# Performance work log

Hardware: AMD Instinct MI355X
Metric: run time of the kernel (lower is better)

Reference implementation:

```python
import jax, jax.numpy as jnp
import numpy as np

T, C, H = 2048, 1024, 16
D = C // H  # head dim = 64


def setup_inputs() -> dict:
    key = jax.random.key(0)
    k1, k2, k3 = jax.random.split(key, 3)
    x = jax.random.normal(k1, (T, C), dtype=jnp.float32)
    W_qkv = jax.random.normal(k2, (C, 3 * C), dtype=jnp.float32) * (1.0 / np.sqrt(C))
    b_qkv = jnp.zeros((3 * C,), dtype=jnp.float32)
    W_proj = jax.random.normal(k3, (C, C), dtype=jnp.float32) * (1.0 / np.sqrt(C))
    b_proj = jnp.zeros((C,), dtype=jnp.float32)
    return {"x": x, "W_qkv": W_qkv, "b_qkv": b_qkv, "W_proj": W_proj, "b_proj": b_proj}


def reference(x, W_qkv, b_qkv, W_proj, b_proj):
    t, c = x.shape
    qkv = x @ W_qkv + b_qkv                      # [T, 3C] fused QKV projection
    q, k, v = jnp.split(qkv, 3, axis=-1)         # each [T, C]
    # split heads: [T, C] -> [H, T, D]
    q = q.reshape(t, H, D).transpose(1, 0, 2)
    k = k.reshape(t, H, D).transpose(1, 0, 2)
    v = v.reshape(t, H, D).transpose(1, 0, 2)
    # naive O(T^2) attention, full score matrix [H, T, T]
    att = jnp.einsum('htd,hsd->hts', q, k) / jnp.sqrt(jnp.float32(D))
    att = jax.nn.softmax(att, axis=-1)
    y = jnp.einsum('hts,hsd->htd', att, v)       # [H, T, D]
    y = y.transpose(1, 0, 2).reshape(t, c)       # merge heads -> [T, C]
    return y @ W_proj + b_proj
```

## Files before the change

kernel.cpp:

```cpp
#include <hip/hip_runtime.h>
#include <hip/hip_bf16.h>
#include <stdint.h>

#define T_DIM 2048
#define C_DIM 1024
#define H_DIM 16
#define D_HEAD 64
#define N_QKV 3072

typedef __bf16 bf16;
typedef __bf16 bf16x8 __attribute__((ext_vector_type(8)));
typedef __bf16 bf16x4 __attribute__((ext_vector_type(4)));
typedef float f32x4 __attribute__((ext_vector_type(4)));

__global__ void cast_bf16_kernel(const float* __restrict__ in, bf16* __restrict__ out, int n) {
    int i = (blockIdx.x * 256 + threadIdx.x) * 8;
    if (i >= n) return;
    float4 a = *(const float4*)(in + i);
    float4 b = *(const float4*)(in + i + 4);
    bf16x8 o;
    o[0] = (bf16)a.x; o[1] = (bf16)a.y; o[2] = (bf16)a.z; o[3] = (bf16)a.w;
    o[4] = (bf16)b.x; o[5] = (bf16)b.y; o[6] = (bf16)b.z; o[7] = (bf16)b.w;
    *(bf16x8*)(out + i) = o;
}

__global__ void cast_transpose_kernel(const float* __restrict__ in, bf16* __restrict__ out,
                                      int K, int N) {
    __shared__ float tile[32][33];
    int kb = blockIdx.y * 32, nb = blockIdx.x * 32;
    int t = threadIdx.x;
    int r = t >> 3, c4 = (t & 7) * 4;
    float4 v = *(const float4*)(in + (size_t)(kb + r) * N + nb + c4);
    tile[r][c4 + 0] = v.x; tile[r][c4 + 1] = v.y;
    tile[r][c4 + 2] = v.z; tile[r][c4 + 3] = v.w;
    __syncthreads();
    bf16x4 ov;
    ov[0] = (bf16)tile[c4 + 0][r]; ov[1] = (bf16)tile[c4 + 1][r];
    ov[2] = (bf16)tile[c4 + 2][r]; ov[3] = (bf16)tile[c4 + 3][r];
    *(bf16x4*)(out + (size_t)(nb + r) * K + kb + c4) = ov;
}

template <typename OutT>
__global__ __launch_bounds__(256, 2) void gemm_bt_kernel(
    const bf16* __restrict__ A, const bf16* __restrict__ Bt,
    const float* __restrict__ bias, OutT* __restrict__ Cmat,
    int M, int N, int K)
{
    __shared__ __align__(16) bf16 As[128][40];
    __shared__ __align__(16) bf16 Bs[128][40];
    int tid  = threadIdx.x;
    int lane = tid & 63, w = tid >> 6;
    int lo16 = lane & 15, quad = lane >> 4;
    int wm = (w & 1) * 64, wn = (w >> 1) * 64;
    int rowBase = blockIdx.y * 128, colBase = blockIdx.x * 128;

    const bf16* aRow = A  + (size_t)(rowBase + (tid >> 1)) * K + (tid & 1) * 16;
    const bf16* bRow = Bt + (size_t)(colBase + (tid >> 1)) * K + (tid & 1) * 16;
    bf16* asDst = &As[tid >> 1][(tid & 1) * 16];
    bf16* bsDst = &Bs[tid >> 1][(tid & 1) * 16];

    f32x4 acc[4][4] = {};

    for (int k0 = 0; k0 < K; k0 += 32) {
        bf16x8 a0 = *(const bf16x8*)(aRow + k0);
        bf16x8 a1 = *(const bf16x8*)(aRow + k0 + 8);
        bf16x8 b0 = *(const bf16x8*)(bRow + k0);
        bf16x8 b1 = *(const bf16x8*)(bRow + k0 + 8);
        __syncthreads();
        *(bf16x8*)asDst = a0; *(bf16x8*)(asDst + 8) = a1;
        *(bf16x8*)bsDst = b0; *(bf16x8*)(bsDst + 8) = b1;
        __syncthreads();
        bf16x8 af[4], bfr[4];
        #pragma unroll
        for (int mi = 0; mi < 4; ++mi) af[mi]  = *(const bf16x8*)&As[wm + mi * 16 + lo16][quad * 8];
        #pragma unroll
        for (int ni = 0; ni < 4; ++ni) bfr[ni] = *(const bf16x8*)&Bs[wn + ni * 16 + lo16][quad * 8];
        #pragma unroll
        for (int mi = 0; mi < 4; ++mi)
            #pragma unroll
            for (int ni = 0; ni < 4; ++ni)
                acc[mi][ni] = __builtin_amdgcn_mfma_f32_16x16x32_bf16(af[mi], bfr[ni], acc[mi][ni], 0, 0, 0);
    }

    #pragma unroll
    for (int ni = 0; ni < 4; ++ni) {
        int col = colBase + wn + ni * 16 + lo16;
        float bv = bias[col];
        #pragma unroll
        for (int mi = 0; mi < 4; ++mi) {
            int row0 = rowBase + wm + mi * 16 + quad * 4;
            #pragma unroll
            for (int r = 0; r < 4; ++r) {
                float v = acc[mi][ni][r] + bv;
                Cmat[(size_t)(row0 + r) * N + col] = (OutT)v;
            }
        }
    }
}

__global__ __launch_bounds__(256, 2) void gemm_bt_128x64_kernel(
    const bf16* __restrict__ A, const bf16* __restrict__ Bt,
    const float* __restrict__ bias, float* __restrict__ Cmat,
    int M, int N, int K)
{
    __shared__ __align__(16) bf16 As[128][40];
    __shared__ __align__(16) bf16 Bs[64][40];
    int tid  = threadIdx.x;
    int lane = tid & 63, w = tid >> 6;
    int lo16 = lane & 15, quad = lane >> 4;
    int wm = (w & 1) * 64, wn = (w >> 1) * 32;
    int rowBase = blockIdx.y * 128, colBase = blockIdx.x * 64;

    const bf16* aRow = A  + (size_t)(rowBase + (tid >> 1)) * K + (tid & 1) * 16;
    const bf16* bRow = Bt + (size_t)(colBase + (tid >> 2)) * K + (tid & 3) * 8;
    bf16* asDst = &As[tid >> 1][(tid & 1) * 16];
    bf16* bsDst = &Bs[tid >> 2][(tid & 3) * 8];

    f32x4 acc[4][2] = {};

    for (int k0 = 0; k0 < K; k0 += 32) {
        bf16x8 a0 = *(const bf16x8*)(aRow + k0);
        bf16x8 a1 = *(const bf16x8*)(aRow + k0 + 8);
        bf16x8 b0 = *(const bf16x8*)(bRow + k0);
        __syncthreads();
        *(bf16x8*)asDst = a0; *(bf16x8*)(asDst + 8) = a1;
        *(bf16x8*)bsDst = b0;
        __syncthreads();
        bf16x8 af[4], bfr[2];
        #pragma unroll
        for (int mi = 0; mi < 4; ++mi) af[mi]  = *(const bf16x8*)&As[wm + mi * 16 + lo16][quad * 8];
        #pragma unroll
        for (int ni = 0; ni < 2; ++ni) bfr[ni] = *(const bf16x8*)&Bs[wn + ni * 16 + lo16][quad * 8];
        #pragma unroll
        for (int mi = 0; mi < 4; ++mi)
            #pragma unroll
            for (int ni = 0; ni < 2; ++ni)
                acc[mi][ni] = __builtin_amdgcn_mfma_f32_16x16x32_bf16(af[mi], bfr[ni], acc[mi][ni], 0, 0, 0);
    }

    #pragma unroll
    for (int ni = 0; ni < 2; ++ni) {
        int col = colBase + wn + ni * 16 + lo16;
        float bv = bias[col];
        #pragma unroll
        for (int mi = 0; mi < 4; ++mi) {
            int row0 = rowBase + wm + mi * 16 + quad * 4;
            #pragma unroll
            for (int r = 0; r < 4; ++r)
                Cmat[(size_t)(row0 + r) * N + col] = acc[mi][ni][r] + bv;
        }
    }
}

__global__ __launch_bounds__(256) void flash_kernel(
    const bf16* __restrict__ qkv,
    bf16* __restrict__ y)
{
    __shared__ __align__(16) bf16 Kd[2][64][40];
    __shared__ __align__(16) bf16 Vt[2][64][40];
    __shared__ __align__(16) bf16 Ps[4][16][72];

    const int h = blockIdx.x, qb = blockIdx.y;
    const int tid  = threadIdx.x;
    const int lane = tid & 63, w = tid >> 6;
    const int lo16 = lane & 15, quad = lane >> 4;
    const int qrow0 = qb * 64 + w * 16;

    bf16x8 qf[2];
    #pragma unroll
    for (int dk = 0; dk < 2; ++dk)
        qf[dk] = *(const bf16x8*)(qkv + (size_t)(qrow0 + lo16) * N_QKV + h * D_HEAD + dk * 32 + quad * 8);

    f32x4 o[4] = {};
    f32x4 l_acc = {};

    const int krow = tid >> 3, kch = tid & 7;
    const int kh = kch >> 2, kc = kch & 3;
    const bf16* kbase = qkv + C_DIM + h * D_HEAD;
    const unsigned short* vbase16 = (const unsigned short*)(qkv + 2 * C_DIM + h * D_HEAD);
    const int vkk = w >> 1, vsb = (w & 1) * 16;

    bf16x8 kreg0, kreg1;
    unsigned short vreg[16];

    {
        const bf16* kp = kbase + (size_t)krow * N_QKV + kch * 8;
        kreg0 = *(const bf16x8*)kp;
        kreg1 = *(const bf16x8*)(kp + (size_t)32 * N_QKV);
        #pragma unroll
        for (int i = 0; i < 16; ++i)
            vreg[i] = vbase16[(size_t)(w * 16 + i) * N_QKV + lane];
    }

    for (int kt = 0; kt < T_DIM / 64; ++kt) {
        __syncthreads();
        *(bf16x8*)&Kd[kh][krow][kc * 8]      = kreg0;
        *(bf16x8*)&Kd[kh][krow + 32][kc * 8] = kreg1;
        union { bf16x8 v; unsigned short u[8]; } p0, p1;
        #pragma unroll
        for (int i = 0; i < 8; ++i) { p0.u[i] = vreg[i]; p1.u[i] = vreg[8 + i]; }
        *(bf16x8*)&Vt[vkk][lane][vsb]     = p0.v;
        *(bf16x8*)&Vt[vkk][lane][vsb + 8] = p1.v;
        __syncthreads();

        if (kt + 1 < T_DIM / 64) {
            const bf16* kp = kbase + (size_t)((kt + 1) * 64 + krow) * N_QKV + kch * 8;
            kreg0 = *(const bf16x8*)kp;
            kreg1 = *(const bf16x8*)(kp + (size_t)32 * N_QKV);
            #pragma unroll
            for (int i = 0; i < 16; ++i)
                vreg[i] = vbase16[(size_t)((kt + 1) * 64 + w * 16 + i) * N_QKV + lane];
        }

        f32x4 s[4] = {};
        #pragma unroll
        for (int dk = 0; dk < 2; ++dk)
            #pragma unroll
            for (int ni = 0; ni < 4; ++ni) {
                bf16x8 kf = *(const bf16x8*)&Kd[dk][ni * 16 + lo16][quad * 8];
                s[ni] = __builtin_amdgcn_mfma_f32_16x16x32_bf16(qf[dk], kf, s[ni], 0, 0, 0);
            }

        #pragma unroll
        for (int ni = 0; ni < 4; ++ni)
            #pragma unroll
            for (int r = 0; r < 4; ++r) {
                float p = __builtin_amdgcn_exp2f(s[ni][r] * 0.18033688011112042f);
                l_acc[r] += p;
                Ps[w][quad * 4 + r][ni * 16 + lo16] = (bf16)p;
            }

        bf16x8 pa0 = *(const bf16x8*)&Ps[w][lo16][quad * 8];
        bf16x8 pa1 = *(const bf16x8*)&Ps[w][lo16][32 + quad * 8];

        #pragma unroll
        for (int ni = 0; ni < 4; ++ni) {
            bf16x8 v0 = *(const bf16x8*)&Vt[0][ni * 16 + lo16][quad * 8];
            o[ni] = __builtin_amdgcn_mfma_f32_16x16x32_bf16(pa0, v0, o[ni], 0, 0, 0);
        }
        #pragma unroll
        for (int ni = 0; ni < 4; ++ni) {
            bf16x8 v1 = *(const bf16x8*)&Vt[1][ni * 16 + lo16][quad * 8];
            o[ni] = __builtin_amdgcn_mfma_f32_16x16x32_bf16(pa1, v1, o[ni], 0, 0, 0);
        }
    }

    #pragma unroll
    for (int off = 1; off < 16; off <<= 1)
        #pragma unroll
        for (int r = 0; r < 4; ++r) l_acc[r] += __shfl_xor(l_acc[r], off);

    f32x4 linv;
    #pragma unroll
    for (int r = 0; r < 4; ++r) linv[r] = 1.0f / l_acc[r];
    #pragma unroll
    for (int ni = 0; ni < 4; ++ni)
        #pragma unroll
        for (int r = 0; r < 4; ++r)
            y[(size_t)(qrow0 + quad * 4 + r) * C_DIM + h * D_HEAD + ni * 16 + lo16] =
                (bf16)(o[ni][r] * linv[r]);
}

extern "C" void kernel_launch(void* const* d_in, const int* in_sizes, int n_in,
                              void* d_out, int out_size, void* d_ws, size_t ws_size,
                              hipStream_t stream) {
    const float* x      = (const float*)d_in[0];
    const float* W_qkv  = (const float*)d_in[1];
    const float* b_qkv  = (const float*)d_in[2];
    const float* W_proj = (const float*)d_in[3];
    const float* b_proj = (const float*)d_in[4];
    float* out = (float*)d_out;

    char* ws = (char*)d_ws;
    bf16* xb      = (bf16*)(ws);
    bf16* Wqkv_t  = (bf16*)(ws + (4  << 20));
    bf16* Wproj_t = (bf16*)(ws + (10 << 20));
    bf16* qkv_bf  = (bf16*)(ws + (12 << 20));
    bf16* yb      = (bf16*)(ws + (24 << 20));

    cast_bf16_kernel<<<(T_DIM * C_DIM) / (256 * 8), 256, 0, stream>>>(x, xb, T_DIM * C_DIM);
    cast_transpose_kernel<<<dim3(N_QKV / 32, C_DIM / 32), 256, 0, stream>>>(W_qkv, Wqkv_t, C_DIM, N_QKV);
    cast_transpose_kernel<<<dim3(C_DIM / 32, C_DIM / 32), 256, 0, stream>>>(W_proj, Wproj_t, C_DIM, C_DIM);

    gemm_bt_kernel<bf16><<<dim3(N_QKV / 128, T_DIM / 128), 256, 0, stream>>>(
        xb, Wqkv_t, b_qkv, qkv_bf, T_DIM, N_QKV, C_DIM);

    flash_kernel<<<dim3(H_DIM, T_DIM / 64), 256, 0, stream>>>(qkv_bf, yb);

    gemm_bt_128x64_kernel<<<dim3(C_DIM / 64, T_DIM / 128), 256, 0, stream>>>(
        yb, Wproj_t, b_proj, out, T_DIM, C_DIM, C_DIM);
}
```

Measured before the change: 174.4 us.

## Split KV in flash attention, add combine pass, use direct-to-LDS GEMM loads

The attention kernel now splits the key/value sequence into two halves across a third grid dimension. It computes transposed S^T and O^T tiles with each wave owning a KV slice, then reduces partial outputs across waves in LDS, and a new combine kernel merges the two halves. Both GEMMs are replaced by a single 128x64 kernel that uses global_load_lds to copy tiles straight into unpadded shared memory. The aim is more parallelism in attention and less register traffic in the GEMMs. The cost is extra partial-output memory traffic, a new kernel launch, and possible LDS bank conflicts from removing the padding.

```diff
diff --git a/kernel.cpp b/kernel.cpp
--- a/kernel.cpp
+++ b/kernel.cpp
@@ -12,6 +12,27 @@
 typedef __bf16 bf16x8 __attribute__((ext_vector_type(8)));
 typedef __bf16 bf16x4 __attribute__((ext_vector_type(4)));
 typedef float f32x4 __attribute__((ext_vector_type(4)));
+typedef short s16x4 __attribute__((ext_vector_type(4)));
+
+__device__ __forceinline__ void lds_load16(const void* g, void* l) {
+    __builtin_amdgcn_global_load_lds(
+        (const __attribute__((address_space(1))) void*)g,
+        (__attribute__((address_space(3))) void*)l, 16, 0, 0);
+}
+
+__device__ __forceinline__ f32x4 mfma16(bf16x4 a, bf16x4 b, f32x4 c) {
+#if __has_builtin(__builtin_amdgcn_mfma_f32_16x16x16_bf16)
+    return __builtin_amdgcn_mfma_f32_16x16x16_bf16(a, b, c, 0, 0, 0);
+#elif __has_builtin(__builtin_amdgcn_mfma_f32_16x16x16bf16_1k)
+    union { bf16x4 v; s16x4 s; } ua, ub;
+    ua.v = a; ub.v = b;
+    return __builtin_amdgcn_mfma_f32_16x16x16bf16_1k(ua.s, ub.s, c, 0, 0, 0);
+#else
+    asm volatile("v_mfma_f32_16x16x16_bf16 %0, %1, %2, %0"
+                 : "+v"(c) : "v"(a), "v"(b));
+    return c;
+#endif
+}
 
 __global__ void cast_bf16_kernel(const float* __restrict__ in, bf16* __restrict__ out, int n) {
     int i = (blockIdx.x * 256 + threadIdx.x) * 8;
@@ -41,90 +62,32 @@
 }
 
 template <typename OutT>
-__global__ __launch_bounds__(256, 2) void gemm_bt_kernel(
+__global__ __launch_bounds__(256) void gemm_lds_kernel(
     const bf16* __restrict__ A, const bf16* __restrict__ Bt,
     const float* __restrict__ bias, OutT* __restrict__ Cmat,
     int M, int N, int K)
 {
-    __shared__ __align__(16) bf16 As[128][40];
-    __shared__ __align__(16) bf16 Bs[128][40];
-    int tid  = threadIdx.x;
-    int lane = tid & 63, w = tid >> 6;
-    int lo16 = lane & 15, quad = lane >> 4;
-    int wm = (w & 1) * 64, wn = (w >> 1) * 64;
-    int rowBase = blockIdx.y * 128, colBase = blockIdx.x * 128;
-
-    const bf16* aRow = A  + (size_t)(rowBase + (tid >> 1)) * K + (tid & 1) * 16;
-    const bf16* bRow = Bt + (size_t)(colBase + (tid >> 1)) * K + (tid & 1) * 16;
-    bf16* asDst = &As[tid >> 1][(tid & 1) * 16];
-    bf16* bsDst = &Bs[tid >> 1][(tid & 1) * 16];
-
-    f32x4 acc[4][4] = {};
-
-    for (int k0 = 0; k0 < K; k0 += 32) {
-        bf16x8 a0 = *(const bf16x8*)(aRow + k0);
-        bf16x8 a1 = *(const bf16x8*)(aRow + k0 + 8);
-        bf16x8 b0 = *(const bf16x8*)(bRow + k0);
-        bf16x8 b1 = *(const bf16x8*)(bRow + k0 + 8);
-        __syncthreads();
-        *(bf16x8*)asDst = a0; *(bf16x8*)(asDst + 8) = a1;
-        *(bf16x8*)bsDst = b0; *(bf16x8*)(bsDst + 8) = b1;
-        __syncthreads();
-        bf16x8 af[4], bfr[4];
-        #pragma unroll
-        for (int mi = 0; mi < 4; ++mi) af[mi]  = *(const bf16x8*)&As[wm + mi * 16 + lo16][quad * 8];
-        #pragma unroll
-        for (int ni = 0; ni < 4; ++ni) bfr[ni] = *(const bf16x8*)&Bs[wn + ni * 16 + lo16][quad * 8];
-        #pragma unroll
-        for (int mi = 0; mi < 4; ++mi)
-            #pragma unroll
-            for (int ni = 0; ni < 4; ++ni)
-                acc[mi][ni] = __builtin_amdgcn_mfma_f32_16x16x32_bf16(af[mi], bfr[ni], acc[mi][ni], 0, 0, 0);
-    }
-
-    #pragma unroll
-    for (int ni = 0; ni < 4; ++ni) {
-        int col = colBase + wn + ni * 16 + lo16;
-        float bv = bias[col];
-        #pragma unroll
-        for (int mi = 0; mi < 4; ++mi) {
-            int row0 = rowBase + wm + mi * 16 + quad * 4;
-            #pragma unroll
-            for (int r = 0; r < 4; ++r) {
-                float v = acc[mi][ni][r] + bv;
-                Cmat[(size_t)(row0 + r) * N + col] = (OutT)v;
-            }
-        }
-    }
-}
-
-__global__ __launch_bounds__(256, 2) void gemm_bt_128x64_kernel(
-    const bf16* __restrict__ A, const bf16* __restrict__ Bt,
-    const float* __restrict__ bias, float* __restrict__ Cmat,
-    int M, int N, int K)
-{
-    __shared__ __align__(16) bf16 As[128][40];
-    __shared__ __align__(16) bf16 Bs[64][40];
+    __shared__ __align__(16) bf16 As[128][32];
+    __shared__ __align__(16) bf16 Bs[64][32];
     int tid  = threadIdx.x;
     int lane = tid & 63, w = tid >> 6;
     int lo16 = lane & 15, quad = lane >> 4;
     int wm = (w & 1) * 64, wn = (w >> 1) * 32;
     int rowBase = blockIdx.y * 128, colBase = blockIdx.x * 64;
 
-    const bf16* aRow = A  + (size_t)(rowBase + (tid >> 1)) * K + (tid & 1) * 16;
-    const bf16* bRow = Bt + (size_t)(colBase + (tid >> 2)) * K + (tid & 3) * 8;
-    bf16* asDst = &As[tid >> 1][(tid & 1) * 16];
-    bf16* bsDst = &Bs[tid >> 2][(tid & 3) * 8];
+    const bf16* ga = A  + (size_t)(rowBase + w * 16 + (lane >> 2)) * K + (lane & 3) * 8;
+    const bf16* gb = Bt + (size_t)(colBase + w * 16 + (lane >> 2)) * K + (lane & 3) * 8;
+    bf16* la0 = &As[w * 16][0];
+    bf16* la1 = &As[64 + w * 16][0];
+    bf16* lb  = &Bs[w * 16][0];
 
     f32x4 acc[4][2] = {};
 
     for (int k0 = 0; k0 < K; k0 += 32) {
-        bf16x8 a0 = *(const bf16x8*)(aRow + k0);
-        bf16x8 a1 = *(const bf16x8*)(aRow + k0 + 8);
-        bf16x8 b0 = *(const bf16x8*)(bRow + k0);
-        __syncthreads();
-        *(bf16x8*)asDst = a0; *(bf16x8*)(asDst + 8) = a1;
-        *(bf16x8*)bsDst = b0;
+        __syncthreads();
+        lds_load16(ga + k0, la0);
+        lds_load16(ga + (size_t)64 * K + k0, la1);
+        lds_load16(gb + k0, lb);
         __syncthreads();
         bf16x8 af[4], bfr[2];
         #pragma unroll
@@ -146,119 +109,158 @@
         for (int mi = 0; mi < 4; ++mi) {
             int row0 = rowBase + wm + mi * 16 + quad * 4;
             #pragma unroll
-            for (int r = 0; r < 4; ++r)
-                Cmat[(size_t)(row0 + r) * N + col] = acc[mi][ni][r] + bv;
-        }
-    }
-}
-
-__global__ __launch_bounds__(256) void flash_kernel(
+            for (int r = 0; r < 4; ++r) {
+                float v = acc[mi][ni][r] + bv;
+                Cmat[(size_t)(row0 + r) * N + col] = (OutT)v;
+            }
+        }
+    }
+}
+
+__global__ __launch_bounds__(256, 3) void flash_kernel(
     const bf16* __restrict__ qkv,
-    bf16* __restrict__ y)
+    bf16* __restrict__ Opart,
+    float* __restrict__ lpart)
 {
-    __shared__ __align__(16) bf16 Kd[2][64][40];
-    __shared__ __align__(16) bf16 Vt[2][64][40];
-    __shared__ __align__(16) bf16 Ps[4][16][72];
-
-    const int h = blockIdx.x, qb = blockIdx.y;
+    __shared__ union {
+        struct {
+            __align__(16) bf16 Kd[2][64][40];
+            __align__(16) bf16 Vt[2][64][40];
+        } t;
+        float Ored[4][16][66];
+    } u;
+    __shared__ float lred[4][64];
+
+    const int h = blockIdx.x, qb = blockIdx.y, sp = blockIdx.z;
     const int tid  = threadIdx.x;
     const int lane = tid & 63, w = tid >> 6;
     const int lo16 = lane & 15, quad = lane >> 4;
-    const int qrow0 = qb * 64 + w * 16;
-
-    bf16x8 qf[2];
-    #pragma unroll
-    for (int dk = 0; dk < 2; ++dk)
-        qf[dk] = *(const bf16x8*)(qkv + (size_t)(qrow0 + lo16) * N_QKV + h * D_HEAD + dk * 32 + quad * 8);
-
-    f32x4 o[4] = {};
-    f32x4 l_acc = {};
+    const int kv0 = sp * (T_DIM / 2);
+
+    bf16x8 qf[4][2];
+    #pragma unroll
+    for (int nq = 0; nq < 4; ++nq)
+        #pragma unroll
+        for (int dk = 0; dk < 2; ++dk)
+            qf[nq][dk] = *(const bf16x8*)(qkv + (size_t)(qb * 64 + nq * 16 + lo16) * N_QKV
+                                          + h * D_HEAD + dk * 32 + quad * 8);
+
+    f32x4 o_t[4][4] = {};
+    float l_acc[4] = {};
 
     const int krow = tid >> 3, kch = tid & 7;
     const int kh = kch >> 2, kc = kch & 3;
     const bf16* kbase = qkv + C_DIM + h * D_HEAD;
-    const unsigned short* vbase16 = (const unsigned short*)(qkv + 2 * C_DIM + h * D_HEAD);
-    const int vkk = w >> 1, vsb = (w & 1) * 16;
+    const unsigned short* vb16 = (const unsigned short*)(qkv + 2 * C_DIM + h * D_HEAD);
 
     bf16x8 kreg0, kreg1;
     unsigned short vreg[16];
-
     {
-        const bf16* kp = kbase + (size_t)krow * N_QKV + kch * 8;
+        const bf16* kp = kbase + (size_t)(kv0 + krow) * N_QKV + kch * 8;
         kreg0 = *(const bf16x8*)kp;
         kreg1 = *(const bf16x8*)(kp + (size_t)32 * N_QKV);
         #pragma unroll
         for (int i = 0; i < 16; ++i)
-            vreg[i] = vbase16[(size_t)(w * 16 + i) * N_QKV + lane];
-    }
-
-    for (int kt = 0; kt < T_DIM / 64; ++kt) {
-        __syncthreads();
-        *(bf16x8*)&Kd[kh][krow][kc * 8]      = kreg0;
-        *(bf16x8*)&Kd[kh][krow + 32][kc * 8] = kreg1;
-        union { bf16x8 v; unsigned short u[8]; } p0, p1;
-        #pragma unroll
-        for (int i = 0; i < 8; ++i) { p0.u[i] = vreg[i]; p1.u[i] = vreg[8 + i]; }
-        *(bf16x8*)&Vt[vkk][lane][vsb]     = p0.v;
-        *(bf16x8*)&Vt[vkk][lane][vsb + 8] = p1.v;
-        __syncthreads();
-
-        if (kt + 1 < T_DIM / 64) {
-            const bf16* kp = kbase + (size_t)((kt + 1) * 64 + krow) * N_QKV + kch * 8;
+            vreg[i] = vb16[(size_t)(kv0 + w * 16 + i) * N_QKV + lane];
+    }
+
+    for (int kt = 0; kt < T_DIM / 2 / 64; ++kt) {
+        __syncthreads();
+        *(bf16x8*)&u.t.Kd[kh][krow][kc * 8]      = kreg0;
+        *(bf16x8*)&u.t.Kd[kh][krow + 32][kc * 8] = kreg1;
+        union { bf16x8 v; unsigned short us[8]; } p0, p1;
+        #pragma unroll
+        for (int i = 0; i < 8; ++i) { p0.us[i] = vreg[i]; p1.us[i] = vreg[8 + i]; }
+        *(bf16x8*)&u.t.Vt[w >> 1][lane][(w & 1) * 16]     = p0.v;
+        *(bf16x8*)&u.t.Vt[w >> 1][lane][(w & 1) * 16 + 8] = p1.v;
+        __syncthreads();
+
+        if (kt + 1 < T_DIM / 2 / 64) {
+            const bf16* kp = kbase + (size_t)(kv0 + (kt + 1) * 64 + krow) * N_QKV + kch * 8;
             kreg0 = *(const bf16x8*)kp;
             kreg1 = *(const bf16x8*)(kp + (size_t)32 * N_QKV);
             #pragma unroll
             for (int i = 0; i < 16; ++i)
-                vreg[i] = vbase16[(size_t)((kt + 1) * 64 + w * 16 + i) * N_QKV + lane];
-        }
-
-        f32x4 s[4] = {};
-        #pragma unroll
-        for (int dk = 0; dk < 2; ++dk)
-            #pragma unroll
-            for (int ni = 0; ni < 4; ++ni) {
-                bf16x8 kf = *(const bf16x8*)&Kd[dk][ni * 16 + lo16][quad * 8];
-                s[ni] = __builtin_amdgcn_mfma_f32_16x16x32_bf16(qf[dk], kf, s[ni], 0, 0, 0);
+                vreg[i] = vb16[(size_t)(kv0 + (kt + 1) * 64 + w * 16 + i) * N_QKV + lane];
+        }
+
+        bf16x8 kf0 = *(const bf16x8*)&u.t.Kd[0][w * 16 + lo16][quad * 8];
+        bf16x8 kf1 = *(const bf16x8*)&u.t.Kd[1][w * 16 + lo16][quad * 8];
+        f32x4 st[4];
+        #pragma unroll
+        for (int nq = 0; nq < 4; ++nq) {
+            f32x4 z = {};
+            z = __builtin_amdgcn_mfma_f32_16x16x32_bf16(kf0, qf[nq][0], z, 0, 0, 0);
+            st[nq] = __builtin_amdgcn_mfma_f32_16x16x32_bf16(kf1, qf[nq][1], z, 0, 0, 0);
+        }
+
+        bf16x4 pb[4];
+        #pragma unroll
+        for (int nq = 0; nq < 4; ++nq)
+            #pragma unroll
+            for (int r = 0; r < 4; ++r) {
+                float p = __builtin_amdgcn_exp2f(st[nq][r] * 0.18033688011112042f);
+                l_acc[nq] += p;
+                pb[nq][r] = (bf16)p;
             }
 
-        #pragma unroll
-        for (int ni = 0; ni < 4; ++ni)
-            #pragma unroll
-            for (int r = 0; r < 4; ++r) {
-                float p = __builtin_amdgcn_exp2f(s[ni][r] * 0.18033688011112042f);
-                l_acc[r] += p;
-                Ps[w][quad * 4 + r][ni * 16 + lo16] = (bf16)p;
-            }
-
-        bf16x8 pa0 = *(const bf16x8*)&Ps[w][lo16][quad * 8];
-        bf16x8 pa1 = *(const bf16x8*)&Ps[w][lo16][32 + quad * 8];
-
-        #pragma unroll
-        for (int ni = 0; ni < 4; ++ni) {
-            bf16x8 v0 = *(const bf16x8*)&Vt[0][ni * 16 + lo16][quad * 8];
-            o[ni] = __builtin_amdgcn_mfma_f32_16x16x32_bf16(pa0, v0, o[ni], 0, 0, 0);
-        }
-        #pragma unroll
-        for (int ni = 0; ni < 4; ++ni) {
-            bf16x8 v1 = *(const bf16x8*)&Vt[1][ni * 16 + lo16][quad * 8];
-            o[ni] = __builtin_amdgcn_mfma_f32_16x16x32_bf16(pa1, v1, o[ni], 0, 0, 0);
-        }
-    }
-
-    #pragma unroll
-    for (int off = 1; off < 16; off <<= 1)
-        #pragma unroll
-        for (int r = 0; r < 4; ++r) l_acc[r] += __shfl_xor(l_acc[r], off);
-
-    f32x4 linv;
-    #pragma unroll
-    for (int r = 0; r < 4; ++r) linv[r] = 1.0f / l_acc[r];
-    #pragma unroll
-    for (int ni = 0; ni < 4; ++ni)
-        #pragma unroll
-        for (int r = 0; r < 4; ++r)
-            y[(size_t)(qrow0 + quad * 4 + r) * C_DIM + h * D_HEAD + ni * 16 + lo16] =
-                (bf16)(o[ni][r] * linv[r]);
+        bf16x4 vf[4];
+        #pragma unroll
+        for (int mi = 0; mi < 4; ++mi)
+            vf[mi] = *(const bf16x4*)&u.t.Vt[w >> 1][mi * 16 + lo16][(w & 1) * 16 + quad * 4];
+
+        #pragma unroll
+        for (int mi = 0; mi < 4; ++mi)
+            #pragma unroll
+            for (int nq = 0; nq < 4; ++nq)
+                o_t[mi][nq] = mfma16(vf[mi], pb[nq], o_t[mi][nq]);
+    }
+
+    #pragma unroll
+    for (int nq = 0; nq < 4; ++nq) {
+        l_acc[nq] += __shfl_xor(l_acc[nq], 16);
+        l_acc[nq] += __shfl_xor(l_acc[nq], 32);
+        if (quad == 0) lred[w][nq * 16 + lo16] = l_acc[nq];
+    }
+    __syncthreads();
+
+    if (tid < 64) {
+        float ls = lred[0][tid] + lred[1][tid] + lred[2][tid] + lred[3][tid];
+        lpart[(size_t)sp * H_DIM * T_DIM + h * T_DIM + qb * 64 + tid] = ls;
+    }
+
+    #pragma unroll
+    for (int mi = 0; mi < 4; ++mi) {
+        #pragma unroll
+        for (int nq = 0; nq < 4; ++nq)
+            #pragma unroll
+            for (int r = 0; r < 4; ++r)
+                u.Ored[w][quad * 4 + r][nq * 16 + lo16] = o_t[mi][nq][r];
+        __syncthreads();
+        int q = tid & 63, dg = tid >> 6;
+        bf16x4 ov;
+        #pragma unroll
+        for (int dj = 0; dj < 4; ++dj) {
+            int d = dg * 4 + dj;
+            ov[dj] = (bf16)(u.Ored[0][d][q] + u.Ored[1][d][q] + u.Ored[2][d][q] + u.Ored[3][d][q]);
+        }
+        *(bf16x4*)&Opart[(size_t)sp * T_DIM * C_DIM + (size_t)(qb * 64 + q) * C_DIM
+                         + h * D_HEAD + mi * 16 + dg * 4] = ov;
+        __syncthreads();
+    }
+}
+
+__global__ void combine_kernel(const bf16* __restrict__ Opart, const float* __restrict__ lpart,
+                               bf16* __restrict__ yb) {
+    int i4 = (blockIdx.x * 256 + threadIdx.x) * 4;
+    int t = i4 >> 10, c = i4 & (C_DIM - 1), h = c >> 6;
+    bf16x4 a = *(const bf16x4*)&Opart[i4];
+    bf16x4 b = *(const bf16x4*)&Opart[(size_t)T_DIM * C_DIM + i4];
+    float li = 1.0f / (lpart[h * T_DIM + t] + lpart[H_DIM * T_DIM + h * T_DIM + t]);
+    bf16x4 o;
+    #pragma unroll
+    for (int j = 0; j < 4; ++j) o[j] = (bf16)(((float)a[j] + (float)b[j]) * li);
+    *(bf16x4*)&yb[i4] = o;
 }
 
 extern "C" void kernel_launch(void* const* d_in, const int* in_sizes, int n_in,
@@ -277,16 +279,20 @@
     bf16* Wproj_t = (bf16*)(ws + (10 << 20));
     bf16* qkv_bf  = (bf16*)(ws + (12 << 20));
     bf16* yb      = (bf16*)(ws + (24 << 20));
+    bf16* Opart   = (bf16*)(ws);
+    float* lpart  = (float*)(ws + (8 << 20));
 
     cast_bf16_kernel<<<(T_DIM * C_DIM) / (256 * 8), 256, 0, stream>>>(x, xb, T_DIM * C_DIM);
     cast_transpose_kernel<<<dim3(N_QKV / 32, C_DIM / 32), 256, 0, stream>>>(W_qkv, Wqkv_t, C_DIM, N_QKV);
     cast_transpose_kernel<<<dim3(C_DIM / 32, C_DIM / 32), 256, 0, stream>>>(W_proj, Wproj_t, C_DIM, C_DIM);
 
-    gemm_bt_kernel<bf16><<<dim3(N_QKV / 128, T_DIM / 128), 256, 0, stream>>>(
+    gemm_lds_kernel<bf16><<<dim3(N_QKV / 64, T_DIM / 128), 256, 0, stream>>>(
         xb, Wqkv_t, b_qkv, qkv_bf, T_DIM, N_QKV, C_DIM);
 
-    flash_kernel<<<dim3(H_DIM, T_DIM / 64), 256, 0, stream>>>(qkv_bf, yb);
-
-    gemm_bt_128x64_kernel<<<dim3(C_DIM / 64, T_DIM / 128), 256, 0, stream>>>(
+    flash_kernel<<<dim3(H_DIM, T_DIM / 64, 2), 256, 0, stream>>>(qkv_bf, Opart, lpart);
+
+    combine_kernel<<<(T_DIM * C_DIM) / (256 * 4), 256, 0, stream>>>(Opart, lpart, yb);
+
+    gemm_lds_kernel<float><<<dim3(C_DIM / 64, T_DIM / 128), 256, 0, stream>>>(
         yb, Wproj_t, b_proj, out, T_DIM, C_DIM, C_DIM);
 }
```

Result: faster. 168.2 us (-3.6%).
